# Optimization experiments

Measured on AMD Instinct MI355X. Metric: run time of the kernel, lower is better.

Reference implementation:

```python
import jax, jax.numpy as jnp
import numpy as np

N, K, D = 100000, 512, 256
DECAY = 0.99


def _cdist(a, b):
    # Euclidean pairwise distance, like torch.cdist (p=2)
    d2 = (jnp.sum(a * a, axis=1)[:, None]
          + jnp.sum(b * b, axis=1)[None, :]
          - 2.0 * a @ b.T)
    return jnp.sqrt(jnp.maximum(d2, 0.0))


def setup_inputs() -> dict:
    key = jax.random.key(0)
    kx, = jax.random.split(key, 1)
    x = jax.random.normal(kx, (N, D), dtype=jnp.float32)
    # 'random' init picks rows of x; using the first K rows guarantees each
    # centroid is its own nearest point -> every cluster non-empty.
    centroids = x[:K]
    # prev_assignments equals the current argmin so the EMA update branch fires
    prev_assignments = jnp.argmin(_cdist(x, centroids), axis=1).astype(jnp.int64)
    return {"x": x, "centroids": centroids, "prev_assignments": prev_assignments}


def reference(x, centroids, prev_assignments):
    distances = _cdist(x, centroids)            # [N, K]
    new_assignments = jnp.argmin(distances, axis=1)  # [N]
    match = jnp.all(new_assignments == prev_assignments)

    def _do_update(_):
        # one-hot scatter accumulation == segment_sum over assignments
        sums = jax.ops.segment_sum(x, new_assignments, num_segments=K)   # [K, D]
        counts = jax.ops.segment_sum(jnp.ones((x.shape[0],), x.dtype),
                                     new_assignments, num_segments=K)    # [K]
        new_c = sums / counts[:, None]
        updated = (1.0 - DECAY) * centroids + DECAY * new_c
        # recompute assignments against updated centroids
        a2 = jnp.argmin(_cdist(x, updated), axis=1)
        return a2, updated, jnp.bool_(True)

    def _no_update(_):
        return new_assignments, centroids, jnp.bool_(False)

    assignments_out, centroids_out, updated_flag = jax.lax.cond(
        match, _do_update, _no_update, None)
    return assignments_out, updated_flag, centroids_out
```

## Files before the change

### kernel.cpp

```cpp
#include <hip/hip_runtime.h>
#include <math.h>

#define DD 256
#define KK 512
#define TM 64
#define TKC 128
#define NCHUNK 4
#define DSL 32
#define NSL 8
#define NSLICES 32
#define SPLIT 4

typedef float float4v __attribute__((ext_vector_type(4)));
typedef float float2v __attribute__((ext_vector_type(2)));

__device__ __forceinline__ void gld_lds16(const void* g, void* l) {
    __builtin_amdgcn_global_load_lds((const __attribute__((address_space(1))) void*)g,
                                     (__attribute__((address_space(3))) void*)l, 16, 0, 0);
}

__global__ __launch_bounds__(256, 2)
void argmin_kernel(const float* __restrict__ x, const float* __restrict__ cent,
                   const float* __restrict__ xx, const float* __restrict__ cc,
                   const int N,
                   int* __restrict__ assign_out,
                   const int* __restrict__ prev, const int pstride,
                   unsigned int* __restrict__ mismatch)
{
    __shared__ float xs[2][TM * DSL];
    __shared__ float cs[2][TKC * DSL];

    const int tid  = threadIdx.x;
    const int w    = tid >> 6;
    const int lane = tid & 63;
    const int tr   = tid >> 4;
    const int tc   = tid & 15;
    const long long rowbase = (long long)blockIdx.x * TM;

    float minv[4]; int mini[4]; float xxr[4];
#pragma unroll
    for (int i = 0; i < 4; ++i) {
        minv[i] = __builtin_inff(); mini[i] = 0;
        int r = (tr << 2) + i;
        long long p = rowbase + r; if (p > N - 1) p = N - 1;
        xxr[i] = xx[p];
    }

    const int r_st  = (w << 3) + (lane >> 3);
    const int slot4 = (lane & 7) << 2;

#define STAGE(BUF, S) do {                                                        \
        const int d0_    = ((S) & 7) * DSL;                                       \
        const int cbase_ = ((S) >> 3) * TKC;                                      \
        _Pragma("unroll")                                                         \
        for (int call = 0; call < 4; ++call) {                                    \
            int r  = (call << 5) + r_st;                                          \
            int dl = slot4 ^ (((r >> 2) & 7) << 2);                               \
            gld_lds16(cent + (long long)(cbase_ + r) * DD + d0_ + dl,             \
                      &cs[(BUF)][((call << 2) + w) << 8]);                        \
            if (call < 2) {                                                       \
                long long p = rowbase + r; if (p > N - 1) p = N - 1;              \
                gld_lds16(x + p * DD + d0_ + dl,                                  \
                          &xs[(BUF)][((call << 2) + w) << 8]);                    \
            }                                                                     \
        }                                                                         \
    } while (0)

    STAGE(0, 0);
    int s = 0;
    float2v acc2[4][8];

#pragma unroll 1
    for (int chunk = 0; chunk < NCHUNK; ++chunk) {
        float ccr[8];
#pragma unroll
        for (int j = 0; j < 8; ++j) {
            int r = ((j >> 2) << 6) + (tc << 2) + (j & 3);
            ccr[j] = cc[chunk * TKC + r];
        }
#pragma unroll
        for (int i = 0; i < 4; ++i)
#pragma unroll
            for (int j = 0; j < 8; ++j) acc2[i][j] = (float2v){0.0f, 0.0f};

#pragma unroll 1
        for (int sl = 0; sl < NSL; ++sl) {
            const int buf = s & 1;
            __syncthreads();
            if (s + 1 < NSLICES) STAGE(buf ^ 1, s + 1);
#pragma unroll
            for (int g = 0; g < 8; ++g) {
                const int dl = g << 2;
                float4v ax[4], bc[8];
#pragma unroll
                for (int i = 0; i < 4; ++i) {
                    int r = (tr << 2) + i;
                    ax[i] = *(const float4v*)&xs[buf][(r << 5) + (dl ^ (((r >> 2) & 7) << 2))];
                }
#pragma unroll
                for (int j = 0; j < 8; ++j) {
                    int r = ((j >> 2) << 6) + (tc << 2) + (j & 3);
                    bc[j] = *(const float4v*)&cs[buf][(r << 5) + (dl ^ (((r >> 2) & 7) << 2))];
                }
#pragma unroll
                for (int i = 0; i < 4; ++i) {
                    const float2v axl = __builtin_shufflevector(ax[i], ax[i], 0, 1);
                    const float2v axh = __builtin_shufflevector(ax[i], ax[i], 2, 3);
#pragma unroll
                    for (int j = 0; j < 8; ++j) {
                        const float2v bcl = __builtin_shufflevector(bc[j], bc[j], 0, 1);
                        const float2v bch = __builtin_shufflevector(bc[j], bc[j], 2, 3);
                        float2v t = acc2[i][j];
                        t = __builtin_elementwise_fma(axl, bcl, t);
                        t = __builtin_elementwise_fma(axh, bch, t);
                        acc2[i][j] = t;
                    }
                }
            }
            ++s;
        }
        {
#pragma clang fp contract(off)
#pragma unroll
            for (int i = 0; i < 4; ++i)
#pragma unroll
                for (int j = 0; j < 8; ++j) {
                    int r = ((j >> 2) << 6) + (tc << 2) + (j & 3);
                    float dot  = acc2[i][j][0] + acc2[i][j][1];
                    float t    = xxr[i] + ccr[j];
                    float d2   = t - 2.0f * dot;
                    float dist = sqrtf(fmaxf(d2, 0.0f));
                    if (dist < minv[i]) { minv[i] = dist; mini[i] = chunk * TKC + r; }
                }
        }
    }
#undef STAGE

#pragma unroll
    for (int i = 0; i < 4; ++i) {
#pragma unroll
        for (int off = 1; off < 16; off <<= 1) {
            float ov = __shfl_xor(minv[i], off);
            int   oi = __shfl_xor(mini[i], off);
            if (ov < minv[i] || (ov == minv[i] && oi < mini[i])) { minv[i] = ov; mini[i] = oi; }
        }
    }
    if (tc == 0) {
        unsigned int mis = 0;
#pragma unroll
        for (int i = 0; i < 4; ++i) {
            long long p = rowbase + (tr << 2) + i;
            if (p < N) {
                assign_out[p] = mini[i];
                if (prev != nullptr && prev[p * pstride] != mini[i]) ++mis;
            }
        }
        if (mis) atomicAdd(mismatch, mis);
    }
}

__global__ void sqnorm_kernel(const float* __restrict__ m, float* __restrict__ out, const int n)
{
    const int w = threadIdx.x >> 6, lane = threadIdx.x & 63;
    const int row = (blockIdx.x << 2) + w;
    if (row >= n) return;
    const float4v v = *(const float4v*)&m[(long long)row * DD + (lane << 2)];
    float s = v[0]*v[0] + v[1]*v[1] + v[2]*v[2] + v[3]*v[3];
#pragma unroll
    for (int off = 1; off < 64; off <<= 1) s += __shfl_xor(s, off);
    if (lane == 0) out[row] = s;
}

__global__ void hist_kernel(const int* __restrict__ assign, int* __restrict__ counts, const int N)
{
    const int p = blockIdx.x * 256 + threadIdx.x;
    if (p < N) atomicAdd(&counts[assign[p]], 1);
}

__global__ __launch_bounds__(KK)
void scan_kernel(const int* __restrict__ counts, int* __restrict__ starts, int* __restrict__ cursor)
{
    __shared__ int buf[2][KK];
    const int t = threadIdx.x;
    const int v = counts[t];
    buf[0][t] = v;
    __syncthreads();
    int src = 0;
#pragma unroll
    for (int off = 1; off < KK; off <<= 1) {
        int val = buf[src][t];
        if (t >= off) val += buf[src][t - off];
        buf[src ^ 1][t] = val;
        src ^= 1;
        __syncthreads();
    }
    const int excl = buf[src][t] - v;
    starts[t] = excl;
    cursor[t] = excl;
}

__global__ void scatter_kernel(const int* __restrict__ assign, int* __restrict__ cursor,
                               int* __restrict__ idx, const int N)
{
    const int p = blockIdx.x * 256 + threadIdx.x;
    if (p >= N) return;
    const int a = assign[p];
    const int pos = atomicAdd(&cursor[a], 1);
    idx[pos] = p;
}

__global__ __launch_bounds__(256)
void gather_kernel(const float* __restrict__ x, const int* __restrict__ idx,
                   const int* __restrict__ starts, const int* __restrict__ counts,
                   unsigned long long* __restrict__ sums)
{
    const int c    = blockIdx.x / SPLIT;
    const int part = blockIdx.x % SPLIT;
    const int d    = threadIdx.x;
    const int start = starts[c], cnt = counts[c];
    const int chunk = (cnt + SPLIT - 1) / SPLIT;
    const int i0 = part * chunk;
    int i1 = i0 + chunk; if (i1 > cnt) i1 = cnt;
    if (i1 <= i0) return;

    long long acc = 0;
    int i = i0;
    for (; i + 4 <= i1; i += 4) {
        const int p0 = idx[start + i + 0];
        const int p1 = idx[start + i + 1];
        const int p2 = idx[start + i + 2];
        const int p3 = idx[start + i + 3];
        const float v0 = x[(long long)p0 * DD + d];
        const float v1 = x[(long long)p1 * DD + d];
        const float v2 = x[(long long)p2 * DD + d];
        const float v3 = x[(long long)p3 * DD + d];
        acc += __double2ll_rn((double)v0 * 1099511627776.0);
        acc += __double2ll_rn((double)v1 * 1099511627776.0);
        acc += __double2ll_rn((double)v2 * 1099511627776.0);
        acc += __double2ll_rn((double)v3 * 1099511627776.0);
    }
    for (; i < i1; ++i) {
        const int p = idx[start + i];
        acc += __double2ll_rn((double)x[(long long)p * DD + d] * 1099511627776.0);
    }
    atomicAdd(&sums[(size_t)c * DD + d], (unsigned long long)acc);
}

__global__ void update_kernel(const float* __restrict__ cent,
                              const unsigned long long* __restrict__ sums,
                              const int* __restrict__ counts,
                              float* __restrict__ updated, float* __restrict__ cc2)
{
    const int c = blockIdx.x, d = threadIdx.x;
    const int w = d >> 6, lane = d & 63;
    __shared__ float red[4];
    float u;
    {
#pragma clang fp contract(off)
        const float cnt = (float)counts[c];
        const float sf  = (float)((double)(long long)sums[(size_t)c * DD + d] * (1.0 / 1099511627776.0));
        const float nc  = sf / cnt;
        u = 0.01f * cent[(size_t)c * DD + d] + 0.99f * nc;
    }
    updated[(size_t)c * DD + d] = u;
    float s = u * u;
#pragma unroll
    for (int off = 1; off < 64; off <<= 1) s += __shfl_xor(s, off);
    if (lane == 0) red[w] = s;
    __syncthreads();
    if (d == 0) cc2[c] = (red[0] + red[1]) + (red[2] + red[3]);
}

__global__ void output_kernel(const unsigned int* __restrict__ mismatch,
                              const int* __restrict__ a1, const int* __restrict__ a2,
                              const float* __restrict__ cent, const float* __restrict__ updated,
                              float* __restrict__ out, const int N, const int total)
{
    const int g = blockIdx.x * 256 + threadIdx.x;
    if (g >= total) return;
    const bool match = (*mismatch == 0u);
    if (g < N)       out[g] = (float)(match ? a2[g] : a1[g]);
    else if (g == N) out[g] = match ? 1.0f : 0.0f;
    else {
        const int e = g - N - 1;
        out[g] = match ? updated[e] : cent[e];
    }
}

extern "C" void kernel_launch(void* const* d_in, const int* in_sizes, int n_in,
                              void* d_out, int out_size, void* d_ws, size_t ws_size,
                              hipStream_t stream)
{
    const float* x    = (const float*)d_in[0];
    const float* cent = (const float*)d_in[1];
    const int*   prev = (const int*)d_in[2];
    const int N = in_sizes[0] / DD;
    const int pstride = (n_in >= 3 && in_sizes[2] >= 2 * N) ? 2 : 1;

    char* ws = (char*)d_ws;
    size_t off = 0;
    auto alloc = [&](size_t b) { void* p = ws + off; off += (b + 255) & ~(size_t)255; return p; };
    int*   assign1 = (int*)alloc((size_t)N * 4);
    int*   assign2 = (int*)alloc((size_t)N * 4);
    float* xx      = (float*)alloc((size_t)N * 4);
    float* cc      = (float*)alloc(KK * 4);
    float* cc2v    = (float*)alloc(KK * 4);
    int*   counts  = (int*)alloc(KK * 4);
    int*   starts  = (int*)alloc(KK * 4);
    int*   cursor  = (int*)alloc(KK * 4);
    int*   idx     = (int*)alloc((size_t)N * 4);
    unsigned long long* sums = (unsigned long long*)alloc((size_t)KK * DD * 8);
    float* updated = (float*)alloc((size_t)KK * DD * 4);
    unsigned int* mismatch = (unsigned int*)alloc(256);

    hipMemsetAsync(counts, 0, KK * 4, stream);
    hipMemsetAsync(sums, 0, (size_t)KK * DD * 8, stream);
    hipMemsetAsync(mismatch, 0, 4, stream);

    sqnorm_kernel<<<(N + 3) / 4, 256, 0, stream>>>(x, xx, N);
    sqnorm_kernel<<<(KK + 3) / 4, 256, 0, stream>>>(cent, cc, KK);

    const int gb = (N + TM - 1) / TM;
    argmin_kernel<<<gb, 256, 0, stream>>>(x, cent, xx, cc, N, assign1, prev, pstride, mismatch);

    hist_kernel<<<(N + 255) / 256, 256, 0, stream>>>(assign1, counts, N);
    scan_kernel<<<1, KK, 0, stream>>>(counts, starts, cursor);
    scatter_kernel<<<(N + 255) / 256, 256, 0, stream>>>(assign1, cursor, idx, N);
    gather_kernel<<<KK * SPLIT, 256, 0, stream>>>(x, idx, starts, counts, sums);

    update_kernel<<<KK, 256, 0, stream>>>(cent, sums, counts, updated, cc2v);

    argmin_kernel<<<gb, 256, 0, stream>>>(x, updated, xx, cc2v, N, assign2, nullptr, 1, nullptr);

    output_kernel<<<(out_size + 255) / 256, 256, 0, stream>>>(mismatch, assign1, assign2,
                                                              cent, updated, (float*)d_out,
                                                              N, out_size);
}
```

Measured before the change: 1.283 ms.

## Drop x norms and sqrt from argmin, fuse histogram into first pass

The argmin now scores each centroid as 0.5*||c||^2 - x·c instead of computing the full sqrt distance. This removes the per-row x squared-norm kernel, its buffer, and the sqrt and fmax work in the epilogue. The cluster-count histogram is folded into the first argmin kernel with atomics, and the gather split factor is raised from 4 to 8. The risk is that ties and rounding can differ from the reference's sqrt-of-clamped-difference, so some assignments may change.

```diff
diff --git a/kernel.cpp b/kernel.cpp
--- a/kernel.cpp
+++ b/kernel.cpp
@@ -9,7 +9,7 @@
 #define DSL 32
 #define NSL 8
 #define NSLICES 32
-#define SPLIT 4
+#define SPLIT 8
 
 typedef float float4v __attribute__((ext_vector_type(4)));
 typedef float float2v __attribute__((ext_vector_type(2)));
@@ -19,13 +19,15 @@
                                      (__attribute__((address_space(3))) void*)l, 16, 0, 0);
 }
 
+template<bool FIRST>
 __global__ __launch_bounds__(256, 2)
 void argmin_kernel(const float* __restrict__ x, const float* __restrict__ cent,
-                   const float* __restrict__ xx, const float* __restrict__ cc,
+                   const float* __restrict__ cc,
                    const int N,
                    int* __restrict__ assign_out,
                    const int* __restrict__ prev, const int pstride,
-                   unsigned int* __restrict__ mismatch)
+                   unsigned int* __restrict__ mismatch,
+                   int* __restrict__ counts)
 {
     __shared__ float xs[2][TM * DSL];
     __shared__ float cs[2][TKC * DSL];
@@ -37,14 +39,9 @@
     const int tc   = tid & 15;
     const long long rowbase = (long long)blockIdx.x * TM;
 
-    float minv[4]; int mini[4]; float xxr[4];
-#pragma unroll
-    for (int i = 0; i < 4; ++i) {
-        minv[i] = __builtin_inff(); mini[i] = 0;
-        int r = (tr << 2) + i;
-        long long p = rowbase + r; if (p > N - 1) p = N - 1;
-        xxr[i] = xx[p];
-    }
+    float minv[4]; int mini[4];
+#pragma unroll
+    for (int i = 0; i < 4; ++i) { minv[i] = __builtin_inff(); mini[i] = 0; }
 
     const int r_st  = (w << 3) + (lane >> 3);
     const int slot4 = (lane & 7) << 2;
@@ -72,11 +69,11 @@
 
 #pragma unroll 1
     for (int chunk = 0; chunk < NCHUNK; ++chunk) {
-        float ccr[8];
+        float cchalf[8];
 #pragma unroll
         for (int j = 0; j < 8; ++j) {
             int r = ((j >> 2) << 6) + (tc << 2) + (j & 3);
-            ccr[j] = cc[chunk * TKC + r];
+            cchalf[j] = 0.5f * cc[chunk * TKC + r];
         }
 #pragma unroll
         for (int i = 0; i < 4; ++i)
@@ -126,11 +123,9 @@
 #pragma unroll
                 for (int j = 0; j < 8; ++j) {
                     int r = ((j >> 2) << 6) + (tc << 2) + (j & 3);
-                    float dot  = acc2[i][j][0] + acc2[i][j][1];
-                    float t    = xxr[i] + ccr[j];
-                    float d2   = t - 2.0f * dot;
-                    float dist = sqrtf(fmaxf(d2, 0.0f));
-                    if (dist < minv[i]) { minv[i] = dist; mini[i] = chunk * TKC + r; }
+                    float dot   = acc2[i][j][0] + acc2[i][j][1];
+                    float score = cchalf[j] - dot;
+                    if (score < minv[i]) { minv[i] = score; mini[i] = chunk * TKC + r; }
                 }
         }
     }
@@ -152,6 +147,9 @@
             long long p = rowbase + (tr << 2) + i;
             if (p < N) {
                 assign_out[p] = mini[i];
+                if (FIRST) {
+                    atomicAdd(&counts[mini[i]], 1);
+                }
                 if (prev != nullptr && prev[p * pstride] != mini[i]) ++mis;
             }
         }
@@ -169,12 +167,6 @@
 #pragma unroll
     for (int off = 1; off < 64; off <<= 1) s += __shfl_xor(s, off);
     if (lane == 0) out[row] = s;
-}
-
-__global__ void hist_kernel(const int* __restrict__ assign, int* __restrict__ counts, const int N)
-{
-    const int p = blockIdx.x * 256 + threadIdx.x;
-    if (p < N) atomicAdd(&counts[assign[p]], 1);
 }
 
 __global__ __launch_bounds__(KK)
@@ -302,7 +294,6 @@
     auto alloc = [&](size_t b) { void* p = ws + off; off += (b + 255) & ~(size_t)255; return p; };
     int*   assign1 = (int*)alloc((size_t)N * 4);
     int*   assign2 = (int*)alloc((size_t)N * 4);
-    float* xx      = (float*)alloc((size_t)N * 4);
     float* cc      = (float*)alloc(KK * 4);
     float* cc2v    = (float*)alloc(KK * 4);
     int*   counts  = (int*)alloc(KK * 4);
@@ -317,20 +308,20 @@
     hipMemsetAsync(sums, 0, (size_t)KK * DD * 8, stream);
     hipMemsetAsync(mismatch, 0, 4, stream);
 
-    sqnorm_kernel<<<(N + 3) / 4, 256, 0, stream>>>(x, xx, N);
     sqnorm_kernel<<<(KK + 3) / 4, 256, 0, stream>>>(cent, cc, KK);
 
     const int gb = (N + TM - 1) / TM;
-    argmin_kernel<<<gb, 256, 0, stream>>>(x, cent, xx, cc, N, assign1, prev, pstride, mismatch);
-
-    hist_kernel<<<(N + 255) / 256, 256, 0, stream>>>(assign1, counts, N);
+    argmin_kernel<true><<<gb, 256, 0, stream>>>(x, cent, cc, N, assign1,
+                                                prev, pstride, mismatch, counts);
+
     scan_kernel<<<1, KK, 0, stream>>>(counts, starts, cursor);
     scatter_kernel<<<(N + 255) / 256, 256, 0, stream>>>(assign1, cursor, idx, N);
     gather_kernel<<<KK * SPLIT, 256, 0, stream>>>(x, idx, starts, counts, sums);
 
     update_kernel<<<KK, 256, 0, stream>>>(cent, sums, counts, updated, cc2v);
 
-    argmin_kernel<<<gb, 256, 0, stream>>>(x, updated, xx, cc2v, N, assign2, nullptr, 1, nullptr);
+    argmin_kernel<false><<<gb, 256, 0, stream>>>(x, updated, cc2v, N, assign2,
+                                                 nullptr, 1, nullptr, nullptr);
 
     output_kernel<<<(out_size + 255) / 256, 256, 0, stream>>>(mismatch, assign1, assign2,
                                                               cent, updated, (float*)d_out,
```

After: 1.042 ms. -18.8%, faster.
